# Optimization experiments

Measured on AMD Instinct MI355X. Metric: run time of the kernel, lower is better.

The kernel has to match this reference:

```python
import math
import jax, jax.numpy as jnp
import numpy as np

FS = 96000.0
N_BIQUADS = 16
HPF_FREQ_RANGE = (20.0, 500.0)
LPF_FREQ_RANGE = (5000.0, 20000.0)
SHELF_FREQ_RANGE = (50.0, 16000.0)
PEAK_FREQ_RANGE = (100.0, 15000.0)
Q_RANGE = (0.5, 16.0)
GAIN_RANGE = (-24.0, 24.0)
BROADBAND_RANGE = (-60.0, 0.0)


def _denorm_log(norm, lo, hi):
    return jnp.exp(math.log(lo) + norm * (math.log(hi) - math.log(lo)))


def _coef_highpass(fc, Q):
    w0 = 2.0 * math.pi * fc / FS
    alpha = jnp.sin(w0) / (2.0 * Q)
    c = jnp.cos(w0)
    b0 = (1 + c) / 2; b1 = -(1 + c); b2 = (1 + c) / 2
    a0 = 1 + alpha; a1 = -2 * c; a2 = 1 - alpha
    return b0 / a0, b1 / a0, b2 / a0, a1 / a0, a2 / a0


def _coef_lowpass(fc, Q):
    w0 = 2.0 * math.pi * fc / FS
    alpha = jnp.sin(w0) / (2.0 * Q)
    c = jnp.cos(w0)
    b0 = (1 - c) / 2; b1 = 1 - c; b2 = (1 - c) / 2
    a0 = 1 + alpha; a1 = -2 * c; a2 = 1 - alpha
    return b0 / a0, b1 / a0, b2 / a0, a1 / a0, a2 / a0


def _coef_lowshelf(fc, gain_db, Q):
    A = 10.0 ** (gain_db / 40.0)
    w0 = 2.0 * math.pi * fc / FS
    alpha = jnp.sin(w0) / (2.0 * Q)
    c = jnp.cos(w0)
    sA = jnp.sqrt(A)
    b0 = A * (A + 1 - (A - 1) * c + 2 * sA * alpha)
    b1 = 2 * A * (A - 1 - (A + 1) * c)
    b2 = A * (A + 1 - (A - 1) * c - 2 * sA * alpha)
    a0 = A + 1 + (A - 1) * c + 2 * sA * alpha
    a1 = -2 * (A - 1 + (A + 1) * c)
    a2 = A + 1 + (A - 1) * c - 2 * sA * alpha
    return b0 / a0, b1 / a0, b2 / a0, a1 / a0, a2 / a0


def _coef_highshelf(fc, gain_db, Q):
    A = 10.0 ** (gain_db / 40.0)
    w0 = 2.0 * math.pi * fc / FS
    alpha = jnp.sin(w0) / (2.0 * Q)
    c = jnp.cos(w0)
    sA = jnp.sqrt(A)
    b0 = A * (A + 1 + (A - 1) * c + 2 * sA * alpha)
    b1 = -2 * A * (A - 1 + (A + 1) * c)
    b2 = A * (A + 1 + (A - 1) * c - 2 * sA * alpha)
    a0 = A + 1 - (A - 1) * c + 2 * sA * alpha
    a1 = 2 * (A - 1 - (A + 1) * c)
    a2 = A + 1 - (A - 1) * c - 2 * sA * alpha
    return b0 / a0, b1 / a0, b2 / a0, a1 / a0, a2 / a0


def _coef_peak(fc, gain_db, Q):
    A = 10.0 ** (gain_db / 40.0)
    w0 = 2.0 * math.pi * fc / FS
    alpha = jnp.sin(w0) / (2.0 * Q)
    c = jnp.cos(w0)
    b0 = 1 + alpha * A; b1 = -2 * c; b2 = 1 - alpha * A
    a0 = 1 + alpha / A; a1 = -2 * c; a2 = 1 - alpha / A
    return b0 / a0, b1 / a0, b2 / a0, a1 / a0, a2 / a0


def _biquad(x, coefs):
    # x: (B, T); coefs: 5 arrays of shape (B,)
    b0, b1, b2, a1, a2 = coefs

    def step(carry, xt):  # xt: (B,)
        s1, s2 = carry
        y = b0 * xt + s1
        return (b1 * xt - a1 * y + s2, b2 * xt - a2 * y), y

    z = jnp.zeros(x.shape[0], x.dtype)
    _, ys = jax.lax.scan(step, (z, z), x.T)  # ys: (T, B)
    return ys.T


def _chain(audio, params):
    B = audio.shape[0]
    bp = params[:, :N_BIQUADS * 3].reshape(B, N_BIQUADS, 3)
    bb_lo, bb_hi = BROADBAND_RANGE
    in_db = bb_lo + params[:, -2] * (bb_hi - bb_lo)
    out_db = bb_lo + params[:, -1] * (bb_hi - bb_lo)
    x = audio * (10.0 ** (in_db / 20.0))[:, None]

    for i in range(N_BIQUADS):
        fn, gn, qn = bp[:, i, 0], bp[:, i, 1], bp[:, i, 2]
        Q = _denorm_log(qn, *Q_RANGE)
        gain = GAIN_RANGE[0] + gn * (GAIN_RANGE[1] - GAIN_RANGE[0])
        if i == 0:  # HPF
            coefs = _coef_highpass(_denorm_log(fn, *HPF_FREQ_RANGE), Q)
        elif i == 15:  # LPF
            coefs = _coef_lowpass(_denorm_log(fn, *LPF_FREQ_RANGE), Q)
        elif i == 1:  # low shelf
            coefs = _coef_lowshelf(_denorm_log(fn, *SHELF_FREQ_RANGE), gain, Q)
        elif i == 14:  # high shelf
            coefs = _coef_highshelf(_denorm_log(fn, *SHELF_FREQ_RANGE), gain, Q)
        else:  # peaking EQ
            coefs = _coef_peak(_denorm_log(fn, *PEAK_FREQ_RANGE), gain, Q)
        x = _biquad(x, coefs)

    return x * (10.0 ** (out_db / 20.0))[:, None]


def setup_inputs() -> dict:
    key = jax.random.key(0)
    k1, k2 = jax.random.split(key)
    audio = jax.random.normal(k1, (16, 262144), dtype=jnp.float32)
    params = jax.random.uniform(k2, (16, 50), dtype=jnp.float32)
    return {"audio": audio, "params": params}


def reference(audio, params):
    return _chain(audio, params)
```

## Files before the change

kernel.cpp:

```cpp
#include <hip/hip_runtime.h>
#include <math.h>

#define BATCH   16
#define T_LEN   262144
#define NB      16
#define L       64
#define GRP     64
#define SUB     16
#define CHAINS  4
#define NSUB    256
#define NSUP    16
#define NG      64
#define NCHUNK  4096
#define XSTRIDE 68

#define DPI 3.14159265358979323846264338327950288

#define OFF_COEF  0
#define OFF_A64   1536
#define OFF_A1K   17920
#define OFF_A16K  34304
#define OFF_QEND  50688
#define OFF_SARR  181760
#define OFF_P     312832

__device__ inline void stage_coefs(int i, double fn, double gn, double qn,
                                   double& B0, double& B1, double& B2,
                                   double& A1, double& A2) {
    const double FS = 96000.0;
    double Q    = exp(log(0.5) + qn * (log(16.0) - log(0.5)));
    double gain = -24.0 + gn * 48.0;
    double lo, hi;
    if (i == 0)            { lo = 20.0;   hi = 500.0;   }
    else if (i == 15)      { lo = 5000.0; hi = 20000.0; }
    else if (i == 1 || i == 14) { lo = 50.0; hi = 16000.0; }
    else                   { lo = 100.0;  hi = 15000.0; }
    double fc    = exp(log(lo) + fn * (log(hi) - log(lo)));
    double w0    = 2.0 * DPI * fc / FS;
    double alpha = sin(w0) / (2.0 * Q);
    double c     = cos(w0);
    double b0, b1, b2, a0, a1, a2;
    if (i == 0) {
        b0 = (1.0 + c) * 0.5; b1 = -(1.0 + c); b2 = (1.0 + c) * 0.5;
        a0 = 1.0 + alpha; a1 = -2.0 * c; a2 = 1.0 - alpha;
    } else if (i == 15) {
        b0 = (1.0 - c) * 0.5; b1 = 1.0 - c; b2 = (1.0 - c) * 0.5;
        a0 = 1.0 + alpha; a1 = -2.0 * c; a2 = 1.0 - alpha;
    } else if (i == 1) {
        double A = pow(10.0, gain / 40.0), sA = sqrt(A);
        b0 = A * ((A + 1.0) - (A - 1.0) * c + 2.0 * sA * alpha);
        b1 = 2.0 * A * ((A - 1.0) - (A + 1.0) * c);
        b2 = A * ((A + 1.0) - (A - 1.0) * c - 2.0 * sA * alpha);
        a0 = (A + 1.0) + (A - 1.0) * c + 2.0 * sA * alpha;
        a1 = -2.0 * ((A - 1.0) + (A + 1.0) * c);
        a2 = (A + 1.0) + (A - 1.0) * c - 2.0 * sA * alpha;
    } else if (i == 14) {
        double A = pow(10.0, gain / 40.0), sA = sqrt(A);
        b0 = A * ((A + 1.0) + (A - 1.0) * c + 2.0 * sA * alpha);
        b1 = -2.0 * A * ((A - 1.0) + (A + 1.0) * c);
        b2 = A * ((A + 1.0) + (A - 1.0) * c - 2.0 * sA * alpha);
        a0 = (A + 1.0) - (A - 1.0) * c + 2.0 * sA * alpha;
        a1 = 2.0 * ((A - 1.0) - (A + 1.0) * c);
        a2 = (A + 1.0) - (A - 1.0) * c - 2.0 * sA * alpha;
    } else {
        double A = pow(10.0, gain / 40.0);
        b0 = 1.0 + alpha * A; b1 = -2.0 * c; b2 = 1.0 - alpha * A;
        a0 = 1.0 + alpha / A; a1 = -2.0 * c; a2 = 1.0 - alpha / A;
    }
    B0 = b0 / a0; B1 = b1 / a0; B2 = b2 / a0; A1 = a1 / a0; A2 = a2 / a0;
}

__global__ __launch_bounds__(256) void k0_setup(const float* __restrict__ params,
                                                float* __restrict__ coefs,
                                                float* __restrict__ A64,
                                                float* __restrict__ A1K,
                                                float* __restrict__ A16K) {
    int b = blockIdx.x;
    int t = threadIdx.x;
    __shared__ double cf[NB][5];
    __shared__ double M1[32 * 32];
    __shared__ double M2[32 * 32];

    if (t < NB) {
        double B0, B1, B2, A1, A2;
        stage_coefs(t, (double)params[b * 50 + t * 3 + 0],
                       (double)params[b * 50 + t * 3 + 1],
                       (double)params[b * 50 + t * 3 + 2], B0, B1, B2, A1, A2);
        float f0 = (float)B0, f1 = (float)B1, f2 = (float)B2, f3 = (float)A1, f4 = (float)A2;
        cf[t][0] = (double)f0; cf[t][1] = (double)f1; cf[t][2] = (double)f2;
        cf[t][3] = (double)f3; cf[t][4] = (double)f4;
        float* cp = coefs + b * 96 + t * 5;
        cp[0] = f0; cp[1] = f1; cp[2] = f2; cp[3] = f3; cp[4] = f4;
    }
    if (t == NB) {
        double indb = -60.0 + (double)params[b * 50 + 48] * 60.0;
        coefs[b * 96 + 80] = (float)pow(10.0, indb / 20.0);
    }
    if (t == NB + 1) {
        double outdb = -60.0 + (double)params[b * 50 + 49] * 60.0;
        coefs[b * 96 + 81] = (float)pow(10.0, outdb / 20.0);
    }
    __syncthreads();

    if (t < 32) {
        double s1[NB], s2[NB];
#pragma unroll
        for (int i = 0; i < NB; i++) {
            s1[i] = (t == 2 * i) ? 1.0 : 0.0;
            s2[i] = (t == 2 * i + 1) ? 1.0 : 0.0;
        }
        double u = 0.0;
#pragma unroll
        for (int i = 0; i < NB; i++) {
            double y  = cf[i][0] * u + s1[i];
            double n1 = cf[i][1] * u - cf[i][3] * y + s2[i];
            double n2 = cf[i][2] * u - cf[i][4] * y;
            s1[i] = n1; s2[i] = n2; u = y;
        }
#pragma unroll
        for (int i = 0; i < NB; i++) {
            M1[(2 * i) * 32 + t]     = s1[i];
            M1[(2 * i + 1) * 32 + t] = s2[i];
        }
    }
    __syncthreads();

    int c  = t & 31;
    int r0 = t >> 5;
    double* src = M1;
    double* dst = M2;
    for (int sq = 0; sq < 14; sq++) {
        double acc[4] = {0.0, 0.0, 0.0, 0.0};
        for (int k = 0; k < 32; k++) {
            double bv = src[k * 32 + c];
#pragma unroll
            for (int e = 0; e < 4; e++)
                acc[e] += src[(e * 8 + r0) * 32 + k] * bv;
        }
#pragma unroll
        for (int e = 0; e < 4; e++) dst[(e * 8 + r0) * 32 + c] = acc[e];
        __syncthreads();
        { double* tmp = src; src = dst; dst = tmp; }
        float* out_m = (sq == 5) ? A64 : (sq == 9) ? A1K : (sq == 13) ? A16K : nullptr;
        if (out_m) {
#pragma unroll
            for (int e = 0; e < 4; e++) {
                int idx = (e * 8 + r0) * 32 + c;
                out_m[b * 1024 + idx] = (float)src[idx];
            }
        }
        __syncthreads();
    }
}

__device__ __forceinline__ float mv_step_rl(const float* ar, float q, float addv) {
    int qi = __float_as_int(q);
    float qb[32];
#pragma unroll
    for (int t = 0; t < 32; t++)
        qb[t] = __int_as_float(__builtin_amdgcn_readlane(qi, t));
    float acc0 = addv, acc1 = 0.f;
#pragma unroll
    for (int t = 0; t < 32; t += 2) {
        acc0 = fmaf(ar[t], qb[t], acc0);
        acc1 = fmaf(ar[t + 1], qb[t + 1], acc1);
    }
    return acc0 + acc1;
}

__device__ __forceinline__ void load_row32(const float* base, int row, float* ar) {
    const float4* a4 = (const float4*)(base + row * 32);
#pragma unroll
    for (int j = 0; j < 8; j++) {
        float4 v = a4[j];
        ar[4 * j + 0] = v.x; ar[4 * j + 1] = v.y;
        ar[4 * j + 2] = v.z; ar[4 * j + 3] = v.w;
    }
}

__device__ __forceinline__ void stage_audio(const float* __restrict__ gbase,
                                            float* __restrict__ xlds, int lane) {
    const float4* g4 = (const float4*)gbase;
    float4 v[16];
#pragma unroll
    for (int it = 0; it < 16; it++) v[it] = g4[it * 64 + lane];
#pragma unroll
    for (int it = 0; it < 16; it++) {
        int idx = it * 64 + lane;
        int ch = idx >> 4, q = idx & 15;
        *(float4*)&xlds[ch * XSTRIDE + q * 4] = v[it];
    }
}

__global__ __launch_bounds__(64, 1) void k1_pass1(const float* __restrict__ audio,
                                                  const float* __restrict__ coefs,
                                                  const float* __restrict__ A64,
                                                  float* __restrict__ P,
                                                  float* __restrict__ Qend) {
    int blk   = blockIdx.x;
    int batch = blk >> 6;
    int grp   = blk & 63;
    int lane  = threadIdx.x;
    int row   = lane & 31;

    __shared__ float xlds[GRP * XSTRIDE];
    __shared__ float plds[GRP][33];

    stage_audio(audio + (size_t)batch * T_LEN + (size_t)grp * GRP * L, xlds, lane);
    __syncthreads();

    const float* cf = coefs + batch * 96;
    float c0[NB], c1[NB], c2[NB], c3[NB], c4[NB];
#pragma unroll
    for (int i = 0; i < NB; i++) {
        c0[i] = cf[i * 5 + 0]; c1[i] = cf[i * 5 + 1]; c2[i] = cf[i * 5 + 2];
        c3[i] = cf[i * 5 + 3]; c4[i] = cf[i * 5 + 4];
    }
    float ing = cf[80];

    float s1[NB], s2[NB];
#pragma unroll
    for (int i = 0; i < NB; i++) { s1[i] = 0.f; s2[i] = 0.f; }

    float* xrow = &xlds[lane * XSTRIDE];
#pragma unroll 1
    for (int tt = 0; tt < 16; tt++) {
        float4 xv = *(const float4*)&xrow[tt * 4];
        float xs[4] = {xv.x, xv.y, xv.z, xv.w};
#pragma unroll
        for (int j = 0; j < 4; j++) {
            float u = ing * xs[j];
#pragma unroll
            for (int i = 0; i < NB; i++) {
                float y  = fmaf(c0[i], u, s1[i]);
                float n1 = fmaf(c1[i], u, s2[i]); n1 = fmaf(-c3[i], y, n1);
                float n2 = c2[i] * u;             n2 = fmaf(-c4[i], y, n2);
                s1[i] = n1; s2[i] = n2; u = y;
            }
        }
    }

    {
        float* pb = P + ((size_t)(batch * NG + grp)) * 2048;
#pragma unroll
        for (int i = 0; i < NB; i++) {
            pb[(2 * i) * 64 + lane]     = s1[i];
            pb[(2 * i + 1) * 64 + lane] = s2[i];
        }
    }

#pragma unroll
    for (int i = 0; i < NB; i++) {
        plds[lane][2 * i]     = s1[i];
        plds[lane][2 * i + 1] = s2[i];
    }
    __syncthreads();

    float ar[32];
    load_row32(A64 + batch * 1024, row, ar);
    float q0 = 0.f, q1 = 0.f, q2 = 0.f, q3 = 0.f;
#pragma unroll 1
    for (int j = 0; j < SUB; j++) {
        float p0 = plds[0 * SUB + j][row];
        float p1 = plds[1 * SUB + j][row];
        float p2 = plds[2 * SUB + j][row];
        float p3 = plds[3 * SUB + j][row];
        q0 = mv_step_rl(ar, q0, p0);
        q1 = mv_step_rl(ar, q1, p1);
        q2 = mv_step_rl(ar, q2, p2);
        q3 = mv_step_rl(ar, q3, p3);
    }
    if (lane < 32) {
        float* qe = Qend + ((size_t)(batch * NSUB + grp * CHAINS)) * 32 + row;
        qe[0] = q0; qe[32] = q1; qe[64] = q2; qe[96] = q3;
    }
}

__global__ __launch_bounds__(256, 1) void k2_combine(const float* __restrict__ A1K,
                                                     const float* __restrict__ A16K,
                                                     const float* __restrict__ Qend,
                                                     float* __restrict__ Sarr) {
    int batch = blockIdx.x;
    int tid   = threadIdx.x;
    int wave  = tid >> 6;
    int lane  = tid & 63;
    int row   = lane & 31;

    __shared__ float qe[NSUB][32];
    __shared__ float qs[NSUP][32];
    __shared__ float ss[NSUP][32];

    {
        const float4* src4 = (const float4*)(Qend + (size_t)batch * NSUB * 32);
        float4* dst4 = (float4*)&qe[0][0];
        for (int i = tid; i < NSUB * 32 / 4; i += 256) dst4[i] = src4[i];
    }
    float ar1k[32];
    load_row32(A1K + batch * 1024, row, ar1k);
    __syncthreads();

    int s0i = wave * 4;
    {
        float q0 = 0.f, q1 = 0.f, q2 = 0.f, q3 = 0.f;
#pragma unroll 1
        for (int j = 0; j < 16; j++) {
            float p0 = qe[(s0i + 0) * 16 + j][row];
            float p1 = qe[(s0i + 1) * 16 + j][row];
            float p2 = qe[(s0i + 2) * 16 + j][row];
            float p3 = qe[(s0i + 3) * 16 + j][row];
            q0 = mv_step_rl(ar1k, q0, p0);
            q1 = mv_step_rl(ar1k, q1, p1);
            q2 = mv_step_rl(ar1k, q2, p2);
            q3 = mv_step_rl(ar1k, q3, p3);
        }
        if (lane < 32) {
            qs[s0i + 0][row] = q0; qs[s0i + 1][row] = q1;
            qs[s0i + 2][row] = q2; qs[s0i + 3][row] = q3;
        }
    }
    __syncthreads();

    if (wave == 0) {
        float ark[32];
        load_row32(A16K + batch * 1024, row, ark);
        float S = 0.f;
#pragma unroll 1
        for (int s = 0; s < NSUP; s++) {
            if (lane < 32) ss[s][row] = S;
            float addv = qs[s][row];
            S = mv_step_rl(ark, S, addv);
        }
    }
    __syncthreads();

    {
        float q0 = ss[s0i + 0][row];
        float q1 = ss[s0i + 1][row];
        float q2 = ss[s0i + 2][row];
        float q3 = ss[s0i + 3][row];
#pragma unroll 1
        for (int j = 0; j < 16; j++) {
            if (lane < 32) {
                Sarr[((size_t)(batch * NSUB + (s0i + 0) * 16 + j)) * 32 + row] = q0;
                Sarr[((size_t)(batch * NSUB + (s0i + 1) * 16 + j)) * 32 + row] = q1;
                Sarr[((size_t)(batch * NSUB + (s0i + 2) * 16 + j)) * 32 + row] = q2;
                Sarr[((size_t)(batch * NSUB + (s0i + 3) * 16 + j)) * 32 + row] = q3;
            }
            float p0 = qe[(s0i + 0) * 16 + j][row];
            float p1 = qe[(s0i + 1) * 16 + j][row];
            float p2 = qe[(s0i + 2) * 16 + j][row];
            float p3 = qe[(s0i + 3) * 16 + j][row];
            q0 = mv_step_rl(ar1k, q0, p0);
            q1 = mv_step_rl(ar1k, q1, p1);
            q2 = mv_step_rl(ar1k, q2, p2);
            q3 = mv_step_rl(ar1k, q3, p3);
        }
    }
}

__global__ __launch_bounds__(64, 1) void k3_pass2(const float* __restrict__ audio,
                                                  const float* __restrict__ coefs,
                                                  const float* __restrict__ A64,
                                                  const float* __restrict__ P,
                                                  const float* __restrict__ Sarr,
                                                  float* __restrict__ out) {
    int blk   = blockIdx.x;
    int batch = blk >> 6;
    int grp   = blk & 63;
    int lane  = threadIdx.x;
    int row   = lane & 31;

    __shared__ float xlds[GRP * XSTRIDE];
    __shared__ float plds[GRP][33];

    stage_audio(audio + (size_t)batch * T_LEN + (size_t)grp * GRP * L, xlds, lane);

    {
        const float* pb = P + ((size_t)(batch * NG + grp)) * 2048;
        float pv[32];
#pragma unroll
        for (int s = 0; s < 32; s++) pv[s] = pb[s * 64 + lane];
#pragma unroll
        for (int s = 0; s < 32; s++) plds[lane][s] = pv[s];
    }
    __syncthreads();

    {
        float ar[32];
        load_row32(A64 + batch * 1024, row, ar);
        const float* sp = Sarr + ((size_t)(batch * NSUB + grp * CHAINS)) * 32 + row;
        float q0 = sp[0], q1 = sp[32], q2 = sp[64], q3 = sp[96];
#pragma unroll 1
        for (int j = 0; j < SUB; j++) {
            float p0 = plds[0 * SUB + j][row];
            float p1 = plds[1 * SUB + j][row];
            float p2 = plds[2 * SUB + j][row];
            float p3 = plds[3 * SUB + j][row];
            if (lane < 32) {
                plds[0 * SUB + j][row] = q0;
                plds[1 * SUB + j][row] = q1;
                plds[2 * SUB + j][row] = q2;
                plds[3 * SUB + j][row] = q3;
            }
            q0 = mv_step_rl(ar, q0, p0);
            q1 = mv_step_rl(ar, q1, p1);
            q2 = mv_step_rl(ar, q2, p2);
            q3 = mv_step_rl(ar, q3, p3);
        }
    }
    __syncthreads();

    const float* cf = coefs + batch * 96;
    float c0[NB], c1[NB], c2[NB], c3[NB], c4[NB];
#pragma unroll
    for (int i = 0; i < NB; i++) {
        c0[i] = cf[i * 5 + 0]; c1[i] = cf[i * 5 + 1]; c2[i] = cf[i * 5 + 2];
        c3[i] = cf[i * 5 + 3]; c4[i] = cf[i * 5 + 4];
    }
    float ing  = cf[80];
    float outg = cf[81];

    float s1[NB], s2[NB];
#pragma unroll
    for (int i = 0; i < NB; i++) {
        s1[i] = plds[lane][2 * i];
        s2[i] = plds[lane][2 * i + 1];
    }

    float* xrow = &xlds[lane * XSTRIDE];
#pragma unroll 1
    for (int tt = 0; tt < 16; tt++) {
        float4 xv = *(const float4*)&xrow[tt * 4];
        float xs[4] = {xv.x, xv.y, xv.z, xv.w};
        float ys[4];
#pragma unroll
        for (int j = 0; j < 4; j++) {
            float u = ing * xs[j];
#pragma unroll
            for (int i = 0; i < NB; i++) {
                float y  = fmaf(c0[i], u, s1[i]);
                float n1 = fmaf(c1[i], u, s2[i]); n1 = fmaf(-c3[i], y, n1);
                float n2 = c2[i] * u;             n2 = fmaf(-c4[i], y, n2);
                s1[i] = n1; s2[i] = n2; u = y;
            }
            ys[j] = outg * u;
        }
        float4 yv; yv.x = ys[0]; yv.y = ys[1]; yv.z = ys[2]; yv.w = ys[3];
        *(float4*)&xrow[tt * 4] = yv;
    }
    __syncthreads();

    {
        float4* g4 = (float4*)(out + (size_t)batch * T_LEN + (size_t)grp * GRP * L);
#pragma unroll
        for (int it = 0; it < 16; it++) {
            int idx = it * 64 + lane;
            int ch = idx >> 4, q = idx & 15;
            g4[it * 64 + lane] = *(const float4*)&xlds[ch * XSTRIDE + q * 4];
        }
    }
}

extern "C" void kernel_launch(void* const* d_in, const int* in_sizes, int n_in,
                              void* d_out, int out_size, void* d_ws, size_t ws_size,
                              hipStream_t stream) {
    const float* audio  = (const float*)d_in[0];
    const float* params = (const float*)d_in[1];
    float* out = (float*)d_out;
    float* ws  = (float*)d_ws;

    float* coefs = ws + OFF_COEF;
    float* A64   = ws + OFF_A64;
    float* A1K   = ws + OFF_A1K;
    float* A16K  = ws + OFF_A16K;
    float* Qend  = ws + OFF_QEND;
    float* Sarr  = ws + OFF_SARR;
    float* P     = ws + OFF_P;

    k0_setup<<<BATCH, 256, 0, stream>>>(params, coefs, A64, A1K, A16K);
    k1_pass1<<<BATCH * NG, 64, 0, stream>>>(audio, coefs, A64, P, Qend);
    k2_combine<<<BATCH, 256, 0, stream>>>(A1K, A16K, Qend, Sarr);
    k3_pass2<<<BATCH * NG, 64, 0, stream>>>(audio, coefs, A64, P, Sarr, out);
}
```

Baseline: 153.3 us.

## Replace second biquad pass with linear state-correction using precomputed impulse matrix

Pass 1 now stores the zero-initial-state output Y0 per chunk, and setup precomputes a 64x32 matrix H that maps initial state to the output response over a 64-sample chunk. The final kernel no longer re-runs the 16-stage biquad recurrence; it adds H times the corrected initial state to Y0 and applies the output gain. This swaps a serial recurrence for a parallel matrix-vector product. The cost is an extra full-size intermediate write and read of Y0, plus some float precision risk from superposition.

```diff
diff --git a/kernel.cpp b/kernel.cpp
--- a/kernel.cpp
+++ b/kernel.cpp
@@ -13,6 +13,7 @@
 #define NG      64
 #define NCHUNK  4096
 #define XSTRIDE 68
+#define PSTRIDE 36
 
 #define DPI 3.14159265358979323846264338327950288
 
@@ -20,9 +21,11 @@
 #define OFF_A64   1536
 #define OFF_A1K   17920
 #define OFF_A16K  34304
-#define OFF_QEND  50688
-#define OFF_SARR  181760
-#define OFF_P     312832
+#define OFF_H     50688
+#define OFF_QEND  83456
+#define OFF_SARR  214528
+#define OFF_P     345600
+#define OFF_Y0    2442752
 
 __device__ inline void stage_coefs(int i, double fn, double gn, double qn,
                                    double& B0, double& B1, double& B2,
@@ -74,12 +77,14 @@
                                                 float* __restrict__ coefs,
                                                 float* __restrict__ A64,
                                                 float* __restrict__ A1K,
-                                                float* __restrict__ A16K) {
+                                                float* __restrict__ A16K,
+                                                float* __restrict__ Hm) {
     int b = blockIdx.x;
     int t = threadIdx.x;
     __shared__ double cf[NB][5];
     __shared__ double M1[32 * 32];
     __shared__ double M2[32 * 32];
+    __shared__ double Hd[64][32];
 
     if (t < NB) {
         double B0, B1, B2, A1, A2;
@@ -122,6 +127,14 @@
             M1[(2 * i) * 32 + t]     = s1[i];
             M1[(2 * i + 1) * 32 + t] = s2[i];
         }
+        Hd[0][t] = u;
+    }
+    __syncthreads();
+
+    if (t < 32) {
+        double a = 0.0;
+        for (int k = 0; k < 32; k++) a += Hd[0][k] * M1[k * 32 + t];
+        Hd[1][t] = a;
     }
     __syncthreads();
 
@@ -149,8 +162,20 @@
                 out_m[b * 1024 + idx] = (float)src[idx];
             }
         }
+        if (sq <= 4) {
+            int m = 2 << sq;
+            for (int idx = t; idx < m * 32; idx += 256) {
+                int r = idx >> 5, cc = idx & 31;
+                double a = 0.0;
+                for (int k = 0; k < 32; k++) a += Hd[r][k] * src[k * 32 + cc];
+                Hd[m + r][cc] = a;
+            }
+        }
         __syncthreads();
     }
+
+    for (int idx = t; idx < 64 * 32; idx += 256)
+        Hm[b * 2048 + idx] = (float)Hd[idx >> 5][idx & 31];
 }
 
 __device__ __forceinline__ float mv_step_rl(const float* ar, float q, float addv) {
@@ -196,7 +221,8 @@
                                                   const float* __restrict__ coefs,
                                                   const float* __restrict__ A64,
                                                   float* __restrict__ P,
-                                                  float* __restrict__ Qend) {
+                                                  float* __restrict__ Qend,
+                                                  float* __restrict__ Y0) {
     int blk   = blockIdx.x;
     int batch = blk >> 6;
     int grp   = blk & 63;
@@ -227,6 +253,7 @@
     for (int tt = 0; tt < 16; tt++) {
         float4 xv = *(const float4*)&xrow[tt * 4];
         float xs[4] = {xv.x, xv.y, xv.z, xv.w};
+        float ys[4];
 #pragma unroll
         for (int j = 0; j < 4; j++) {
             float u = ing * xs[j];
@@ -237,7 +264,10 @@
                 float n2 = c2[i] * u;             n2 = fmaf(-c4[i], y, n2);
                 s1[i] = n1; s2[i] = n2; u = y;
             }
-        }
+            ys[j] = u;
+        }
+        float4 yv; yv.x = ys[0]; yv.y = ys[1]; yv.z = ys[2]; yv.w = ys[3];
+        *(float4*)&xrow[tt * 4] = yv;
     }
 
     {
@@ -255,6 +285,16 @@
         plds[lane][2 * i + 1] = s2[i];
     }
     __syncthreads();
+
+    {
+        float4* g4 = (float4*)(Y0 + (size_t)batch * T_LEN + (size_t)grp * GRP * L);
+#pragma unroll
+        for (int it = 0; it < 16; it++) {
+            int idx = it * 64 + lane;
+            int ch = idx >> 4, q = idx & 15;
+            g4[it * 64 + lane] = *(const float4*)&xlds[ch * XSTRIDE + q * 4];
+        }
+    }
 
     float ar[32];
     load_row32(A64 + batch * 1024, row, ar);
@@ -358,12 +398,13 @@
     }
 }
 
-__global__ __launch_bounds__(64, 1) void k3_pass2(const float* __restrict__ audio,
-                                                  const float* __restrict__ coefs,
-                                                  const float* __restrict__ A64,
-                                                  const float* __restrict__ P,
-                                                  const float* __restrict__ Sarr,
-                                                  float* __restrict__ out) {
+__global__ __launch_bounds__(64, 1) void k3_correct(const float* __restrict__ coefs,
+                                                    const float* __restrict__ A64,
+                                                    const float* __restrict__ Hm,
+                                                    const float* __restrict__ P,
+                                                    const float* __restrict__ Sarr,
+                                                    const float* __restrict__ Y0,
+                                                    float* __restrict__ out) {
     int blk   = blockIdx.x;
     int batch = blk >> 6;
     int grp   = blk & 63;
@@ -371,9 +412,9 @@
     int row   = lane & 31;
 
     __shared__ float xlds[GRP * XSTRIDE];
-    __shared__ float plds[GRP][33];
-
-    stage_audio(audio + (size_t)batch * T_LEN + (size_t)grp * GRP * L, xlds, lane);
+    __shared__ float plds[GRP][PSTRIDE];
+
+    stage_audio(Y0 + (size_t)batch * T_LEN + (size_t)grp * GRP * L, xlds, lane);
 
     {
         const float* pb = P + ((size_t)(batch * NG + grp)) * 2048;
@@ -381,7 +422,11 @@
 #pragma unroll
         for (int s = 0; s < 32; s++) pv[s] = pb[s * 64 + lane];
 #pragma unroll
-        for (int s = 0; s < 32; s++) plds[lane][s] = pv[s];
+        for (int m = 0; m < 8; m++) {
+            float4 v; v.x = pv[4 * m]; v.y = pv[4 * m + 1];
+            v.z = pv[4 * m + 2]; v.w = pv[4 * m + 3];
+            *(float4*)&plds[lane][4 * m] = v;
+        }
     }
     __syncthreads();
 
@@ -410,43 +455,24 @@
     }
     __syncthreads();
 
-    const float* cf = coefs + batch * 96;
-    float c0[NB], c1[NB], c2[NB], c3[NB], c4[NB];
-#pragma unroll
-    for (int i = 0; i < NB; i++) {
-        c0[i] = cf[i * 5 + 0]; c1[i] = cf[i * 5 + 1]; c2[i] = cf[i * 5 + 2];
-        c3[i] = cf[i * 5 + 3]; c4[i] = cf[i * 5 + 4];
-    }
-    float ing  = cf[80];
-    float outg = cf[81];
-
-    float s1[NB], s2[NB];
-#pragma unroll
-    for (int i = 0; i < NB; i++) {
-        s1[i] = plds[lane][2 * i];
-        s2[i] = plds[lane][2 * i + 1];
-    }
-
-    float* xrow = &xlds[lane * XSTRIDE];
-#pragma unroll 1
-    for (int tt = 0; tt < 16; tt++) {
-        float4 xv = *(const float4*)&xrow[tt * 4];
-        float xs[4] = {xv.x, xv.y, xv.z, xv.w};
-        float ys[4];
-#pragma unroll
-        for (int j = 0; j < 4; j++) {
-            float u = ing * xs[j];
-#pragma unroll
-            for (int i = 0; i < NB; i++) {
-                float y  = fmaf(c0[i], u, s1[i]);
-                float n1 = fmaf(c1[i], u, s2[i]); n1 = fmaf(-c3[i], y, n1);
-                float n2 = c2[i] * u;             n2 = fmaf(-c4[i], y, n2);
-                s1[i] = n1; s2[i] = n2; u = y;
+    {
+        float hr[32];
+        load_row32(Hm + batch * 2048, lane, hr);
+        float outg = coefs[batch * 96 + 81];
+#pragma unroll 2
+        for (int ch = 0; ch < GRP; ch++) {
+            float a0 = 0.f, a1 = 0.f;
+#pragma unroll
+            for (int m = 0; m < 8; m++) {
+                float4 s = *(const float4*)&plds[ch][4 * m];
+                a0 = fmaf(hr[4 * m + 0], s.x, a0);
+                a1 = fmaf(hr[4 * m + 1], s.y, a1);
+                a0 = fmaf(hr[4 * m + 2], s.z, a0);
+                a1 = fmaf(hr[4 * m + 3], s.w, a1);
             }
-            ys[j] = outg * u;
-        }
-        float4 yv; yv.x = ys[0]; yv.y = ys[1]; yv.z = ys[2]; yv.w = ys[3];
-        *(float4*)&xrow[tt * 4] = yv;
+            float y0v = xlds[ch * XSTRIDE + lane];
+            xlds[ch * XSTRIDE + lane] = outg * (y0v + a0 + a1);
+        }
     }
     __syncthreads();
 
@@ -473,12 +499,14 @@
     float* A64   = ws + OFF_A64;
     float* A1K   = ws + OFF_A1K;
     float* A16K  = ws + OFF_A16K;
+    float* Hm    = ws + OFF_H;
     float* Qend  = ws + OFF_QEND;
     float* Sarr  = ws + OFF_SARR;
     float* P     = ws + OFF_P;
-
-    k0_setup<<<BATCH, 256, 0, stream>>>(params, coefs, A64, A1K, A16K);
-    k1_pass1<<<BATCH * NG, 64, 0, stream>>>(audio, coefs, A64, P, Qend);
+    float* Y0    = ws + OFF_Y0;
+
+    k0_setup<<<BATCH, 256, 0, stream>>>(params, coefs, A64, A1K, A16K, Hm);
+    k1_pass1<<<BATCH * NG, 64, 0, stream>>>(audio, coefs, A64, P, Qend, Y0);
     k2_combine<<<BATCH, 256, 0, stream>>>(A1K, A16K, Qend, Sarr);
-    k3_pass2<<<BATCH * NG, 64, 0, stream>>>(audio, coefs, A64, P, Sarr, out);
-}
+    k3_correct<<<BATCH * NG, 64, 0, stream>>>(coefs, A64, Hm, P, Sarr, Y0, out);
+}
```

Measured after the change: 166.8 us. +8.9%, slower.
